# Kernel tuning notes

Measured on AMD Instinct MI355X. Metric: run time of the kernel, lower is better.

The kernel has to match this reference:

```python
import jax, jax.numpy as jnp
import numpy as np

EPS = 1e-12
NUM_ITERATIONS = 3


def squash(t, axis=-1):
    sn = jnp.sum(t * t, axis=axis, keepdims=True)
    scale = sn / (1.0 + sn + EPS)
    return scale * t / jnp.sqrt(sn + EPS)


def setup_inputs() -> dict:
    key = jax.random.key(0)
    k1, k2 = jax.random.split(key)
    B, R, IN, OUT, C = 128, 4096, 16, 32, 2
    x = jax.random.normal(k1, (B, R, IN), dtype=jnp.float32)
    # learned parameter: torch.randn(num_capsules, num_route_nodes, in, out)
    route_weights = jax.random.normal(k2, (C, R, IN, OUT), dtype=jnp.float32)
    return {"x": x, "route_weights": route_weights}


def reference(x, route_weights):
    # priors: [C, B, R, 1, O] == x[None,:,:,None,:] @ W[:,None,:,:,:]
    priors = jnp.einsum('bri,crio->cbro', x, route_weights)[..., None, :]
    # logits kept [C,B,R,1,1]: the torch code stores [C,B,R,1,O] but every
    # update (delta_logits) is constant along O, so softmax over axis=2 is identical.
    logits = jnp.zeros(priors.shape[:-1] + (1,), dtype=priors.dtype)
    outputs = None
    for i in range(NUM_ITERATIONS):
        probs = jax.nn.softmax(logits, axis=2)                      # over route nodes
        s = jnp.sum(probs * priors, axis=2, keepdims=True)          # [C,B,1,1,O]
        outputs = squash(s, axis=-1)
        if i != NUM_ITERATIONS - 1:
            delta = jnp.sum(priors * outputs, axis=-1, keepdims=True)  # [C,B,R,1,1]
            logits = logits + delta
    return outputs
```

## Files before the change

kernel.cpp:

```cpp
#include <hip/hip_runtime.h>
#include <math.h>

#define CB    128
#define CR    4096
#define CIN   16
#define COUT  32
#define CCAP  2
#define RC    16
#define NRCH  (CR / RC)
#define EPSF  1e-12f

typedef _Float16 h8  __attribute__((ext_vector_type(8)));
typedef float    f4  __attribute__((ext_vector_type(4)));

__global__ __launch_bounds__(256) void caps_prepack_kernel(
    const float* __restrict__ w, h8* __restrict__ wp)
{
  const int blk = (int)blockIdx.x;
  const int c   = blk >> 10;
  const int r0  = (blk & 1023) * 4;
  const int t   = (int)threadIdx.x;

  __shared__ __align__(16) float Wl[4 * 512];
  {
    const float4* src = (const float4*)(w + ((size_t)c * CR + r0) * 512);
    ((float4*)Wl)[t]       = src[t];
    ((float4*)Wl)[t + 256] = src[t + 256];
  }
  __syncthreads();

  const int rr = t >> 6;
  const int L  = t & 63;
  const int g  = L >> 4, m = L & 15;
  h8 v;
#pragma unroll
  for (int j = 0; j < 4; ++j) {
    v[j]     = (_Float16)Wl[rr * 512 + (4 * g + j) * 32 + m];
    v[4 + j] = (_Float16)Wl[rr * 512 + (4 * g + j) * 32 + 16 + m];
  }
  wp[((size_t)c * CR + r0 + rr) * 64 + L] = v;
}

__device__ __forceinline__ void store_partials(float* __restrict__ partialA,
                                               float* __restrict__ partialE,
                                               const float* accA, const float* accB,
                                               float esum, int c, int rch,
                                               int t, int g, int b)
{
  float4 a4 = {accA[0], accA[1], accA[2], accA[3]};
  float4 b4 = {accB[0], accB[1], accB[2], accB[3]};
  float* dst = partialA + ((size_t)(c * NRCH + rch)) * 4096 + (size_t)t * 8;
  *(float4*)dst = a4;
  *(float4*)(dst + 4) = b4;
  if (g == 0) partialE[((size_t)(c * NRCH + rch)) * CB + b] = esum;
}

__global__ __launch_bounds__(512) void caps_pass_kernel(
    const float* __restrict__ x, const h8* __restrict__ wp,
    const float* __restrict__ vsum,
    float* __restrict__ partialA, float* __restrict__ partialE,
    int uniform)
{
  const int blk = (int)blockIdx.x;
  const int c = blk >> 8, rch = blk & 255;
  const int r0 = rch * RC;
  const int t = (int)threadIdx.x;
  const int wv = t >> 6, L = t & 63, g = L >> 4, m = L & 15;
  const int b  = wv * 16 + m;

  const h8* wrow = wp + ((size_t)c * CR + r0) * 64 + L;
  const float* xrow = x + ((size_t)b * CR + r0) * CIN + 4 * g;

  float4 vA = {0.f, 0.f, 0.f, 0.f}, vB = {0.f, 0.f, 0.f, 0.f};
  if (!uniform) {
    const float* vb = vsum + ((size_t)c * CB + b) * COUT;
    vA = *(const float4*)(vb + 4 * g);
    vB = *(const float4*)(vb + 16 + 4 * g);
  }

  float accA[4] = {0.f, 0.f, 0.f, 0.f};
  float accB[4] = {0.f, 0.f, 0.f, 0.f};
  float esum = 0.f;

#pragma unroll 4
  for (int ri = 0; ri < RC; ++ri) {
    float4 xf = *(const float4*)(xrow + ri * CIN);
    h8 bx = {(_Float16)xf.x, (_Float16)xf.y, (_Float16)xf.z, (_Float16)xf.w,
             (_Float16)0.f, (_Float16)0.f, (_Float16)0.f, (_Float16)0.f};
    h8 wf = wrow[ri * 64];
    h8 aA = {wf[0], wf[1], wf[2], wf[3],
             (_Float16)0.f, (_Float16)0.f, (_Float16)0.f, (_Float16)0.f};
    h8 aB = {wf[4], wf[5], wf[6], wf[7],
             (_Float16)0.f, (_Float16)0.f, (_Float16)0.f, (_Float16)0.f};
    f4 z = {0.f, 0.f, 0.f, 0.f};
    f4 pA = __builtin_amdgcn_mfma_f32_16x16x32_f16(aA, bx, z, 0, 0, 0);
    f4 pB = __builtin_amdgcn_mfma_f32_16x16x32_f16(aB, bx, z, 0, 0, 0);

    float e = 1.f;
    if (!uniform) {
      float d = pA[0] * vA.x + pA[1] * vA.y + pA[2] * vA.z + pA[3] * vA.w
              + pB[0] * vB.x + pB[1] * vB.y + pB[2] * vB.z + pB[3] * vB.w;
      d += __shfl_xor(d, 16);
      d += __shfl_xor(d, 32);
      e = __expf(d);
    }
    esum += e;
#pragma unroll
    for (int j = 0; j < 4; ++j) { accA[j] += e * pA[j]; accB[j] += e * pB[j]; }
  }
  store_partials(partialA, partialE, accA, accB, esum, c, rch, t, g, b);
}

__global__ __launch_bounds__(256) void caps_redv_kernel(
    const float* __restrict__ partialA, const float* __restrict__ partialE,
    float* __restrict__ vsum, float* __restrict__ out, int mode)
{
  const int cb = (int)blockIdx.x;
  const int c2 = cb >> 7, b2 = cb & 127;
  const int t  = (int)threadIdx.x;
  const int o = t & 31, jg = t >> 5;
  const int wv2 = b2 >> 4, m2 = b2 & 15;
  const int half = o >> 4, oo = o & 15, g2 = oo >> 2, j2 = oo & 3;
  const size_t idx = (size_t)(wv2 * 64 + g2 * 16 + m2) * 8 + half * 4 + j2;

  __shared__ float red[8][33];
  __shared__ float rede[8];

  float s = 0.f;
#pragma unroll 4
  for (int k = 0; k < NRCH / 8; ++k) {
    const int j = jg + k * 8;
    s += partialA[((size_t)(c2 * NRCH + j)) * 4096 + idx];
  }
  red[jg][o] = s;
  __syncthreads();

  if (t < 8) {
    float e = 0.f;
#pragma unroll 4
    for (int k = 0; k < NRCH / 8; ++k)
      e += partialE[((size_t)(c2 * NRCH + t + k * 8)) * CB + b2];
    rede[t] = e;
  }
  __syncthreads();

  if (t < 32) {
    float sv = 0.f, es = 0.f;
#pragma unroll
    for (int jj = 0; jj < 8; ++jj) { sv += red[jj][t]; es += rede[jj]; }
    float sm = sv / es;
    float sn = sm * sm;
#pragma unroll
    for (int sh = 1; sh < 32; sh <<= 1) sn += __shfl_xor(sn, sh);
    float fac = sn / ((1.f + sn + EPSF) * sqrtf(sn + EPSF));
    float vv = sm * fac;
    if (mode == 2)      out[cb * COUT + t]  = vv;
    else if (mode == 1) vsum[cb * COUT + t] += vv;
    else                vsum[cb * COUT + t] = vv;
  }
}

extern "C" void kernel_launch(void* const* d_in, const int* in_sizes, int n_in,
                              void* d_out, int out_size, void* d_ws, size_t ws_size,
                              hipStream_t stream) {
  const float* x = (const float*)d_in[0];
  const float* w = (const float*)d_in[1];
  float* out = (float*)d_out;

  char* p = (char*)d_ws;
  h8* wp = (h8*)p;
  p += (size_t)CCAP * CR * 64 * sizeof(h8);
  float* vsum = (float*)p;
  p += (size_t)CCAP * CB * COUT * sizeof(float);
  float* partialA = (float*)p;
  p += (size_t)CCAP * NRCH * 4096 * sizeof(float);
  float* partialE = (float*)p;

  caps_prepack_kernel<<<dim3(CCAP * 1024), 256, 0, stream>>>(w, wp);
  caps_pass_kernel<<<dim3(CCAP * NRCH), 512, 0, stream>>>(
      x, wp, vsum, partialA, partialE, 1);
  caps_redv_kernel<<<dim3(CCAP * CB), 256, 0, stream>>>(
      partialA, partialE, vsum, out, 0);
  caps_pass_kernel<<<dim3(CCAP * NRCH), 512, 0, stream>>>(
      x, wp, vsum, partialA, partialE, 0);
  caps_redv_kernel<<<dim3(CCAP * CB), 256, 0, stream>>>(
      partialA, partialE, vsum, out, 1);
  caps_pass_kernel<<<dim3(CCAP * NRCH), 512, 0, stream>>>(
      x, wp, vsum, partialA, partialE, 0);
  caps_redv_kernel<<<dim3(CCAP * CB), 256, 0, stream>>>(
      partialA, partialE, vsum, out, 2);
}
```

Baseline: 78.77 us.

## Prepack x to fp16 lane layout and process both capsules per block

Adds a kernel that converts x once to fp16 in the exact per-lane MFMA layout, so each of the three routing passes reads half the bytes with coalesced 8-byte loads. Each pass block now computes both capsules and reuses the same x fragment for both weight sets, which halves x traffic again. The route chunk shrinks from 16 to 8, keeping the block count unchanged. In exchange there is an extra launch and more workspace, and the partial buffers double in size, so the reduce kernels have twice as many partials to sum.

```diff
diff --git a/kernel.cpp b/kernel.cpp
--- a/kernel.cpp
+++ b/kernel.cpp
@@ -1,19 +1,20 @@
 #include <hip/hip_runtime.h>
 #include <math.h>
 
-#define CB    128
-#define CR    4096
-#define CIN   16
-#define COUT  32
-#define CCAP  2
-#define RC    16
-#define NRCH  (CR / RC)
-#define EPSF  1e-12f
+#define CB     128
+#define CR     4096
+#define CIN    16
+#define COUT   32
+#define CCAP   2
+#define RC     8
+#define NRCH2  (CR / RC)
+#define EPSF   1e-12f
 
 typedef _Float16 h8  __attribute__((ext_vector_type(8)));
+typedef _Float16 h4t __attribute__((ext_vector_type(4)));
 typedef float    f4  __attribute__((ext_vector_type(4)));
 
-__global__ __launch_bounds__(256) void caps_prepack_kernel(
+__global__ __launch_bounds__(256) void caps_prepw_kernel(
     const float* __restrict__ w, h8* __restrict__ wp)
 {
   const int blk = (int)blockIdx.x;
@@ -41,6 +42,25 @@
   wp[((size_t)c * CR + r0 + rr) * 64 + L] = v;
 }
 
+__global__ __launch_bounds__(256) void caps_prepx_kernel(
+    const float* __restrict__ x, h4t* __restrict__ xq)
+{
+  const int G  = (int)(blockIdx.x * 256 + threadIdx.x);
+  const int g  = G & 3;
+  const int wv = (G >> 2) & 7;
+  const int r  = G >> 5;
+
+  h4t recs[16];
+#pragma unroll
+  for (int m = 0; m < 16; ++m) {
+    float4 xf = *(const float4*)(x + ((size_t)(wv * 16 + m) * CR + r) * CIN + 4 * g);
+    recs[m] = h4t{(_Float16)xf.x, (_Float16)xf.y, (_Float16)xf.z, (_Float16)xf.w};
+  }
+  h4t* dst = xq + ((size_t)(r * 8 + wv)) * 64 + g * 16;
+#pragma unroll
+  for (int m = 0; m < 16; ++m) dst[m] = recs[m];
+}
+
 __device__ __forceinline__ void store_partials(float* __restrict__ partialA,
                                                float* __restrict__ partialE,
                                                const float* accA, const float* accB,
@@ -49,66 +69,83 @@
 {
   float4 a4 = {accA[0], accA[1], accA[2], accA[3]};
   float4 b4 = {accB[0], accB[1], accB[2], accB[3]};
-  float* dst = partialA + ((size_t)(c * NRCH + rch)) * 4096 + (size_t)t * 8;
+  float* dst = partialA + ((size_t)(c * NRCH2 + rch)) * 4096 + (size_t)t * 8;
   *(float4*)dst = a4;
   *(float4*)(dst + 4) = b4;
-  if (g == 0) partialE[((size_t)(c * NRCH + rch)) * CB + b] = esum;
-}
-
-__global__ __launch_bounds__(512) void caps_pass_kernel(
-    const float* __restrict__ x, const h8* __restrict__ wp,
+  if (g == 0) partialE[((size_t)(c * NRCH2 + rch)) * CB + b] = esum;
+}
+
+__global__ __launch_bounds__(512, 4) void caps_pass_kernel(
+    const h4t* __restrict__ xq, const h8* __restrict__ wp,
     const float* __restrict__ vsum,
     float* __restrict__ partialA, float* __restrict__ partialE,
     int uniform)
 {
-  const int blk = (int)blockIdx.x;
-  const int c = blk >> 8, rch = blk & 255;
-  const int r0 = rch * RC;
-  const int t = (int)threadIdx.x;
-  const int wv = t >> 6, L = t & 63, g = L >> 4, m = L & 15;
-  const int b  = wv * 16 + m;
-
-  const h8* wrow = wp + ((size_t)c * CR + r0) * 64 + L;
-  const float* xrow = x + ((size_t)b * CR + r0) * CIN + 4 * g;
-
-  float4 vA = {0.f, 0.f, 0.f, 0.f}, vB = {0.f, 0.f, 0.f, 0.f};
+  const int rch = (int)blockIdx.x;
+  const int r0  = rch * RC;
+  const int t   = (int)threadIdx.x;
+  const int wv  = t >> 6, L = t & 63, g = L >> 4, m = L & 15;
+  const int b   = wv * 16 + m;
+
+  const h4t* xrow  = xq + ((size_t)(r0 * 8 + wv)) * 64 + L;
+  const h8*  w0row = wp + ((size_t)0 * CR + r0) * 64 + L;
+  const h8*  w1row = wp + ((size_t)1 * CR + r0) * 64 + L;
+
+  float4 vA0 = {0.f,0.f,0.f,0.f}, vB0 = {0.f,0.f,0.f,0.f};
+  float4 vA1 = {0.f,0.f,0.f,0.f}, vB1 = {0.f,0.f,0.f,0.f};
   if (!uniform) {
-    const float* vb = vsum + ((size_t)c * CB + b) * COUT;
-    vA = *(const float4*)(vb + 4 * g);
-    vB = *(const float4*)(vb + 16 + 4 * g);
-  }
-
-  float accA[4] = {0.f, 0.f, 0.f, 0.f};
-  float accB[4] = {0.f, 0.f, 0.f, 0.f};
-  float esum = 0.f;
-
-#pragma unroll 4
+    const float* vb0 = vsum + ((size_t)0 * CB + b) * COUT;
+    vA0 = *(const float4*)(vb0 + 4 * g);
+    vB0 = *(const float4*)(vb0 + 16 + 4 * g);
+    const float* vb1 = vsum + ((size_t)1 * CB + b) * COUT;
+    vA1 = *(const float4*)(vb1 + 4 * g);
+    vB1 = *(const float4*)(vb1 + 16 + 4 * g);
+  }
+
+  float acc0A[4] = {0.f,0.f,0.f,0.f}, acc0B[4] = {0.f,0.f,0.f,0.f};
+  float acc1A[4] = {0.f,0.f,0.f,0.f}, acc1B[4] = {0.f,0.f,0.f,0.f};
+  float esum0 = 0.f, esum1 = 0.f;
+
+#pragma unroll
   for (int ri = 0; ri < RC; ++ri) {
-    float4 xf = *(const float4*)(xrow + ri * CIN);
-    h8 bx = {(_Float16)xf.x, (_Float16)xf.y, (_Float16)xf.z, (_Float16)xf.w,
+    h4t xr = xrow[ri * 512];
+    h8 bx = {xr[0], xr[1], xr[2], xr[3],
              (_Float16)0.f, (_Float16)0.f, (_Float16)0.f, (_Float16)0.f};
-    h8 wf = wrow[ri * 64];
-    h8 aA = {wf[0], wf[1], wf[2], wf[3],
-             (_Float16)0.f, (_Float16)0.f, (_Float16)0.f, (_Float16)0.f};
-    h8 aB = {wf[4], wf[5], wf[6], wf[7],
-             (_Float16)0.f, (_Float16)0.f, (_Float16)0.f, (_Float16)0.f};
+    h8 wf0 = w0row[ri * 64];
+    h8 wf1 = w1row[ri * 64];
+    h8 aA0 = {wf0[0], wf0[1], wf0[2], wf0[3],
+              (_Float16)0.f, (_Float16)0.f, (_Float16)0.f, (_Float16)0.f};
+    h8 aB0 = {wf0[4], wf0[5], wf0[6], wf0[7],
+              (_Float16)0.f, (_Float16)0.f, (_Float16)0.f, (_Float16)0.f};
+    h8 aA1 = {wf1[0], wf1[1], wf1[2], wf1[3],
+              (_Float16)0.f, (_Float16)0.f, (_Float16)0.f, (_Float16)0.f};
+    h8 aB1 = {wf1[4], wf1[5], wf1[6], wf1[7],
+              (_Float16)0.f, (_Float16)0.f, (_Float16)0.f, (_Float16)0.f};
     f4 z = {0.f, 0.f, 0.f, 0.f};
-    f4 pA = __builtin_amdgcn_mfma_f32_16x16x32_f16(aA, bx, z, 0, 0, 0);
-    f4 pB = __builtin_amdgcn_mfma_f32_16x16x32_f16(aB, bx, z, 0, 0, 0);
-
-    float e = 1.f;
+    f4 pA0 = __builtin_amdgcn_mfma_f32_16x16x32_f16(aA0, bx, z, 0, 0, 0);
+    f4 pB0 = __builtin_amdgcn_mfma_f32_16x16x32_f16(aB0, bx, z, 0, 0, 0);
+    f4 pA1 = __builtin_amdgcn_mfma_f32_16x16x32_f16(aA1, bx, z, 0, 0, 0);
+    f4 pB1 = __builtin_amdgcn_mfma_f32_16x16x32_f16(aB1, bx, z, 0, 0, 0);
+
+    float e0 = 1.f, e1 = 1.f;
     if (!uniform) {
-      float d = pA[0] * vA.x + pA[1] * vA.y + pA[2] * vA.z + pA[3] * vA.w
-              + pB[0] * vB.x + pB[1] * vB.y + pB[2] * vB.z + pB[3] * vB.w;
-      d += __shfl_xor(d, 16);
-      d += __shfl_xor(d, 32);
-      e = __expf(d);
+      float d0 = pA0[0]*vA0.x + pA0[1]*vA0.y + pA0[2]*vA0.z + pA0[3]*vA0.w
+               + pB0[0]*vB0.x + pB0[1]*vB0.y + pB0[2]*vB0.z + pB0[3]*vB0.w;
+      float d1 = pA1[0]*vA1.x + pA1[1]*vA1.y + pA1[2]*vA1.z + pA1[3]*vA1.w
+               + pB1[0]*vB1.x + pB1[1]*vB1.y + pB1[2]*vB1.z + pB1[3]*vB1.w;
+      d0 += __shfl_xor(d0, 16);  d1 += __shfl_xor(d1, 16);
+      d0 += __shfl_xor(d0, 32);  d1 += __shfl_xor(d1, 32);
+      e0 = __expf(d0);           e1 = __expf(d1);
     }
-    esum += e;
-#pragma unroll
-    for (int j = 0; j < 4; ++j) { accA[j] += e * pA[j]; accB[j] += e * pB[j]; }
-  }
-  store_partials(partialA, partialE, accA, accB, esum, c, rch, t, g, b);
+    esum0 += e0;  esum1 += e1;
+#pragma unroll
+    for (int j = 0; j < 4; ++j) {
+      acc0A[j] += e0 * pA0[j];  acc0B[j] += e0 * pB0[j];
+      acc1A[j] += e1 * pA1[j];  acc1B[j] += e1 * pB1[j];
+    }
+  }
+  store_partials(partialA, partialE, acc0A, acc0B, esum0, 0, rch, t, g, b);
+  store_partials(partialA, partialE, acc1A, acc1B, esum1, 1, rch, t, g, b);
 }
 
 __global__ __launch_bounds__(256) void caps_redv_kernel(
@@ -127,19 +164,19 @@
   __shared__ float rede[8];
 
   float s = 0.f;
-#pragma unroll 4
-  for (int k = 0; k < NRCH / 8; ++k) {
+#pragma unroll 8
+  for (int k = 0; k < NRCH2 / 8; ++k) {
     const int j = jg + k * 8;
-    s += partialA[((size_t)(c2 * NRCH + j)) * 4096 + idx];
+    s += partialA[((size_t)(c2 * NRCH2 + j)) * 4096 + idx];
   }
   red[jg][o] = s;
   __syncthreads();
 
   if (t < 8) {
     float e = 0.f;
-#pragma unroll 4
-    for (int k = 0; k < NRCH / 8; ++k)
-      e += partialE[((size_t)(c2 * NRCH + t + k * 8)) * CB + b2];
+#pragma unroll 8
+    for (int k = 0; k < NRCH2 / 8; ++k)
+      e += partialE[((size_t)(c2 * NRCH2 + t + k * 8)) * CB + b2];
     rede[t] = e;
   }
   __syncthreads();
@@ -170,23 +207,26 @@
   char* p = (char*)d_ws;
   h8* wp = (h8*)p;
   p += (size_t)CCAP * CR * 64 * sizeof(h8);
+  h4t* xq = (h4t*)p;
+  p += (size_t)CR * 8 * 64 * sizeof(h4t);
   float* vsum = (float*)p;
   p += (size_t)CCAP * CB * COUT * sizeof(float);
   float* partialA = (float*)p;
-  p += (size_t)CCAP * NRCH * 4096 * sizeof(float);
+  p += (size_t)CCAP * NRCH2 * 4096 * sizeof(float);
   float* partialE = (float*)p;
 
-  caps_prepack_kernel<<<dim3(CCAP * 1024), 256, 0, stream>>>(w, wp);
-  caps_pass_kernel<<<dim3(CCAP * NRCH), 512, 0, stream>>>(
-      x, wp, vsum, partialA, partialE, 1);
+  caps_prepw_kernel<<<dim3(CCAP * 1024), 256, 0, stream>>>(w, wp);
+  caps_prepx_kernel<<<dim3(512), 256, 0, stream>>>(x, xq);
+  caps_pass_kernel<<<dim3(NRCH2), 512, 0, stream>>>(
+      xq, wp, vsum, partialA, partialE, 1);
   caps_redv_kernel<<<dim3(CCAP * CB), 256, 0, stream>>>(
       partialA, partialE, vsum, out, 0);
-  caps_pass_kernel<<<dim3(CCAP * NRCH), 512, 0, stream>>>(
-      x, wp, vsum, partialA, partialE, 0);
+  caps_pass_kernel<<<dim3(NRCH2), 512, 0, stream>>>(
+      xq, wp, vsum, partialA, partialE, 0);
   caps_redv_kernel<<<dim3(CCAP * CB), 256, 0, stream>>>(
       partialA, partialE, vsum, out, 1);
-  caps_pass_kernel<<<dim3(CCAP * NRCH), 512, 0, stream>>>(
-      x, wp, vsum, partialA, partialE, 0);
+  caps_pass_kernel<<<dim3(NRCH2), 512, 0, stream>>>(
+      xq, wp, vsum, partialA, partialE, 0);
   caps_redv_kernel<<<dim3(CCAP * CB), 256, 0, stream>>>(
       partialA, partialE, vsum, out, 2);
 }
```

After: 143.8 us. 1.83x slower.

## Prepack x into fp16 route-major layout and halve route chunk size

Applied to the files above, without the earlier changes.

Adds a kernel that converts x to fp16 and transposes it once into a route-major layout, so each pass kernel reads coalesced 8-byte fp16 records instead of strided fp32 rows. The route chunk per block drops from 16 to 8, which doubles the block count, and occupancy is raised with launch bounds. Together these aim to cut the memory traffic in the three pass kernels and improve parallelism. In exchange there is an extra transpose kernel, more partial buffers for the reduction kernel to sum, and the existing fp16 x rounding now happens in a separate step.

```diff
diff --git a/kernel.cpp b/kernel.cpp
--- a/kernel.cpp
+++ b/kernel.cpp
@@ -1,19 +1,20 @@
 #include <hip/hip_runtime.h>
 #include <math.h>
 
-#define CB    128
-#define CR    4096
-#define CIN   16
-#define COUT  32
-#define CCAP  2
-#define RC    16
-#define NRCH  (CR / RC)
-#define EPSF  1e-12f
+#define CB     128
+#define CR     4096
+#define CIN    16
+#define COUT   32
+#define CCAP   2
+#define RC     8
+#define NRCH2  (CR / RC)
+#define EPSF   1e-12f
 
 typedef _Float16 h8  __attribute__((ext_vector_type(8)));
+typedef _Float16 h4t __attribute__((ext_vector_type(4)));
 typedef float    f4  __attribute__((ext_vector_type(4)));
 
-__global__ __launch_bounds__(256) void caps_prepack_kernel(
+__global__ __launch_bounds__(256) void caps_prepw_kernel(
     const float* __restrict__ w, h8* __restrict__ wp)
 {
   const int blk = (int)blockIdx.x;
@@ -41,6 +42,49 @@
   wp[((size_t)c * CR + r0 + rr) * 64 + L] = v;
 }
 
+#define XL(bb, rr_, ii) ((bb) * 1105 + (rr_) * 17 + (ii))
+__global__ __launch_bounds__(256) void caps_prepx_kernel(
+    const float* __restrict__ x, h4t* __restrict__ xq)
+{
+  const int blk = (int)blockIdx.x;
+  const int wv  = blk >> 6;
+  const int rch = blk & 63;
+  const int r0  = rch * 64;
+  const int t   = (int)threadIdx.x;
+
+  __shared__ float Xl[16 * 65 * 17];
+
+  {
+    const int brow = t >> 4, chunk = t & 15;
+    const float4* src = (const float4*)(
+        x + ((size_t)(wv * 16 + brow)) * CR * CIN + (size_t)r0 * CIN);
+#pragma unroll
+    for (int k = 0; k < 16; ++k) {
+      const int fi = chunk + k * 16;
+      float4 v = src[fi];
+      const int rl = fi >> 2, iq = fi & 3;
+      float* d = &Xl[XL(brow, rl, iq * 4)];
+      d[0] = v.x; d[1] = v.y; d[2] = v.z; d[3] = v.w;
+    }
+  }
+  __syncthreads();
+
+  {
+    const int rl = t >> 2, g = t & 3;
+    h4t recs[16];
+#pragma unroll
+    for (int m = 0; m < 16; ++m) {
+      recs[m] = h4t{(_Float16)Xl[XL(m, rl, 4 * g + 0)],
+                    (_Float16)Xl[XL(m, rl, 4 * g + 1)],
+                    (_Float16)Xl[XL(m, rl, 4 * g + 2)],
+                    (_Float16)Xl[XL(m, rl, 4 * g + 3)]};
+    }
+    h4t* dst = xq + ((size_t)(r0 + rl) * 8 + wv) * 64 + g * 16;
+#pragma unroll
+    for (int m = 0; m < 16; ++m) dst[m] = recs[m];
+  }
+}
+
 __device__ __forceinline__ void store_partials(float* __restrict__ partialA,
                                                float* __restrict__ partialE,
                                                const float* accA, const float* accB,
@@ -49,27 +93,27 @@
 {
   float4 a4 = {accA[0], accA[1], accA[2], accA[3]};
   float4 b4 = {accB[0], accB[1], accB[2], accB[3]};
-  float* dst = partialA + ((size_t)(c * NRCH + rch)) * 4096 + (size_t)t * 8;
+  float* dst = partialA + ((size_t)(c * NRCH2 + rch)) * 4096 + (size_t)t * 8;
   *(float4*)dst = a4;
   *(float4*)(dst + 4) = b4;
-  if (g == 0) partialE[((size_t)(c * NRCH + rch)) * CB + b] = esum;
-}
-
-__global__ __launch_bounds__(512) void caps_pass_kernel(
-    const float* __restrict__ x, const h8* __restrict__ wp,
+  if (g == 0) partialE[((size_t)(c * NRCH2 + rch)) * CB + b] = esum;
+}
+
+__global__ __launch_bounds__(512, 4) void caps_pass_kernel(
+    const h4t* __restrict__ xq, const h8* __restrict__ wp,
     const float* __restrict__ vsum,
     float* __restrict__ partialA, float* __restrict__ partialE,
     int uniform)
 {
   const int blk = (int)blockIdx.x;
-  const int c = blk >> 8, rch = blk & 255;
+  const int c = blk >> 9, rch = blk & 511;
   const int r0 = rch * RC;
   const int t = (int)threadIdx.x;
   const int wv = t >> 6, L = t & 63, g = L >> 4, m = L & 15;
   const int b  = wv * 16 + m;
 
-  const h8* wrow = wp + ((size_t)c * CR + r0) * 64 + L;
-  const float* xrow = x + ((size_t)b * CR + r0) * CIN + 4 * g;
+  const h4t* xrow = xq + ((size_t)(r0 * 8 + wv)) * 64 + L;
+  const h8*  wrow = wp + ((size_t)c * CR + r0) * 64 + L;
 
   float4 vA = {0.f, 0.f, 0.f, 0.f}, vB = {0.f, 0.f, 0.f, 0.f};
   if (!uniform) {
@@ -82,10 +126,10 @@
   float accB[4] = {0.f, 0.f, 0.f, 0.f};
   float esum = 0.f;
 
-#pragma unroll 4
+#pragma unroll
   for (int ri = 0; ri < RC; ++ri) {
-    float4 xf = *(const float4*)(xrow + ri * CIN);
-    h8 bx = {(_Float16)xf.x, (_Float16)xf.y, (_Float16)xf.z, (_Float16)xf.w,
+    h4t xr = xrow[ri * 512];
+    h8 bx = {xr[0], xr[1], xr[2], xr[3],
              (_Float16)0.f, (_Float16)0.f, (_Float16)0.f, (_Float16)0.f};
     h8 wf = wrow[ri * 64];
     h8 aA = {wf[0], wf[1], wf[2], wf[3],
@@ -127,19 +171,19 @@
   __shared__ float rede[8];
 
   float s = 0.f;
-#pragma unroll 4
-  for (int k = 0; k < NRCH / 8; ++k) {
+#pragma unroll 8
+  for (int k = 0; k < NRCH2 / 8; ++k) {
     const int j = jg + k * 8;
-    s += partialA[((size_t)(c2 * NRCH + j)) * 4096 + idx];
+    s += partialA[((size_t)(c2 * NRCH2 + j)) * 4096 + idx];
   }
   red[jg][o] = s;
   __syncthreads();
 
   if (t < 8) {
     float e = 0.f;
-#pragma unroll 4
-    for (int k = 0; k < NRCH / 8; ++k)
-      e += partialE[((size_t)(c2 * NRCH + t + k * 8)) * CB + b2];
+#pragma unroll 8
+    for (int k = 0; k < NRCH2 / 8; ++k)
+      e += partialE[((size_t)(c2 * NRCH2 + t + k * 8)) * CB + b2];
     rede[t] = e;
   }
   __syncthreads();
@@ -170,23 +214,26 @@
   char* p = (char*)d_ws;
   h8* wp = (h8*)p;
   p += (size_t)CCAP * CR * 64 * sizeof(h8);
+  h4t* xq = (h4t*)p;
+  p += (size_t)CR * 8 * 64 * sizeof(h4t);
   float* vsum = (float*)p;
   p += (size_t)CCAP * CB * COUT * sizeof(float);
   float* partialA = (float*)p;
-  p += (size_t)CCAP * NRCH * 4096 * sizeof(float);
+  p += (size_t)CCAP * NRCH2 * 4096 * sizeof(float);
   float* partialE = (float*)p;
 
-  caps_prepack_kernel<<<dim3(CCAP * 1024), 256, 0, stream>>>(w, wp);
-  caps_pass_kernel<<<dim3(CCAP * NRCH), 512, 0, stream>>>(
-      x, wp, vsum, partialA, partialE, 1);
+  caps_prepw_kernel<<<dim3(CCAP * 1024), 256, 0, stream>>>(w, wp);
+  caps_prepx_kernel<<<dim3(512), 256, 0, stream>>>(x, xq);
+  caps_pass_kernel<<<dim3(CCAP * NRCH2), 512, 0, stream>>>(
+      xq, wp, vsum, partialA, partialE, 1);
   caps_redv_kernel<<<dim3(CCAP * CB), 256, 0, stream>>>(
       partialA, partialE, vsum, out, 0);
-  caps_pass_kernel<<<dim3(CCAP * NRCH), 512, 0, stream>>>(
-      x, wp, vsum, partialA, partialE, 0);
+  caps_pass_kernel<<<dim3(CCAP * NRCH2), 512, 0, stream>>>(
+      xq, wp, vsum, partialA, partialE, 0);
   caps_redv_kernel<<<dim3(CCAP * CB), 256, 0, stream>>>(
       partialA, partialE, vsum, out, 1);
-  caps_pass_kernel<<<dim3(CCAP * NRCH), 512, 0, stream>>>(
-      x, wp, vsum, partialA, partialE, 0);
+  caps_pass_kernel<<<dim3(CCAP * NRCH2), 512, 0, stream>>>(
+      xq, wp, vsum, partialA, partialE, 0);
   caps_redv_kernel<<<dim3(CCAP * CB), 256, 0, stream>>>(
       partialA, partialE, vsum, out, 2);
 }
```

After: 106.3 us. +34.9%, slower.
